# Optimization experiments

Hardware: AMD Instinct MI355X
Metric: run time of the kernel (lower is better)

The kernel has to match this reference:

```python
import jax, jax.numpy as jnp
import numpy as np
import math

B, S, D, H, FF, V, L = 8, 1024, 512, 8, 2048, 32000, 6
HD = D // H
EPS = 1e-6


def _positional_encoding(seq_len, d_model):
    pos = np.arange(seq_len, dtype=np.float32)[:, None]
    div = np.exp(np.arange(0, d_model, 2, dtype=np.float32) * (-math.log(10000.0) / d_model))
    pe = np.zeros((seq_len, d_model), dtype=np.float32)
    pe[:, 0::2] = np.sin(pos * div)
    pe[:, 1::2] = np.cos(pos * div)
    return jnp.asarray(pe)[None]  # [1, S, D]


def setup_inputs() -> dict:
    key = jax.random.key(0)
    ks = jax.random.split(key, 10)
    s = 0.02
    return {
        'tokens': jax.random.randint(ks[0], (B, S), 0, V, dtype=jnp.int32),
        'mask': jnp.ones((B, 1, 1, S), dtype=jnp.int32),
        'emb': jax.random.normal(ks[1], (V, D), jnp.float32) * s,
        'Wq': jax.random.normal(ks[2], (D, D), jnp.float32) * s,
        'bq': jnp.zeros((D,), jnp.float32),
        'Wk': jax.random.normal(ks[3], (D, D), jnp.float32) * s,
        'bk': jnp.zeros((D,), jnp.float32),
        'Wv': jax.random.normal(ks[4], (D, D), jnp.float32) * s,
        'bv': jnp.zeros((D,), jnp.float32),
        'Wo': jax.random.normal(ks[5], (D, D), jnp.float32) * s,
        'bo': jnp.zeros((D,), jnp.float32),
        'W1': jax.random.normal(ks[6], (D, FF), jnp.float32) * s,
        'b1': jnp.zeros((FF,), jnp.float32),
        'W2': jax.random.normal(ks[7], (FF, D), jnp.float32) * s,
        'b2': jnp.zeros((D,), jnp.float32),
        'ln_a1': jnp.ones((1,), jnp.float32),
        'ln_b1': jnp.zeros((1,), jnp.float32),
        'ln_a2': jnp.ones((1,), jnp.float32),
        'ln_b2': jnp.zeros((1,), jnp.float32),
    }


def _layernorm(x, alpha, bias):
    # custom LN from source: unbiased std (torch default), scalar alpha/bias,
    # eps added to std (not variance)
    mean = jnp.mean(x, axis=-1, keepdims=True)
    std = jnp.std(x, axis=-1, keepdims=True, ddof=1)
    return alpha * (x - mean) / (std + EPS) + bias


def reference(tokens, mask, emb, Wq, bq, Wk, bk, Wv, bv, Wo, bo,
              W1, b1, W2, b2, ln_a1, ln_b1, ln_a2, ln_b2):
    b, s = tokens.shape
    x = emb[tokens] * jnp.asarray(math.sqrt(D), emb.dtype)  # [B,S,D]
    x = x + _positional_encoding(s, D)
    neg = jnp.asarray(-1e9, x.dtype)
    scale = jnp.asarray(1.0 / math.sqrt(HD), x.dtype)
    # NOTE: source reuses the same EncoderBlock instance -> shared weights per layer
    for _ in range(L):
        # --- self-attention sublayer (pre-norm residual) ---
        h = _layernorm(x, ln_a1, ln_b1)
        q = (h @ Wq + bq).reshape(b, s, H, HD).transpose(0, 2, 1, 3)
        k = (h @ Wk + bk).reshape(b, s, H, HD).transpose(0, 2, 1, 3)
        v = (h @ Wv + bv).reshape(b, s, H, HD).transpose(0, 2, 1, 3)
        scores = jnp.einsum('bhqd,bhkd->bhqk', q, k) * scale
        scores = jnp.where(mask == 0, neg, scores)
        attn = jax.nn.softmax(scores, axis=-1)
        o = jnp.einsum('bhqk,bhkd->bhqd', attn, v)
        o = o.transpose(0, 2, 1, 3).reshape(b, s, D)
        x = x + (o @ Wo + bo)
        # --- feed-forward sublayer (pre-norm residual) ---
        h2 = _layernorm(x, ln_a2, ln_b2)
        x = x + (jax.nn.relu(h2 @ W1 + b1) @ W2 + b2)
    return x
```

## Files before the change

### kernel.cpp

```cpp
#include <hip/hip_runtime.h>
#include <hip/hip_bf16.h>
#include <math.h>

#define BB 8
#define SS 1024
#define DD 512
#define HH 8
#define FF 2048
#define LL 6
#define HD 64
#define MM (BB * SS)
#define EPS 1e-6f
#define QKVS 1536

typedef __attribute__((ext_vector_type(8))) short bf16x8;
typedef __attribute__((ext_vector_type(4))) float f32x4;

typedef __attribute__((address_space(1))) const unsigned int g_u32;
typedef __attribute__((address_space(3))) unsigned int l_u32;

__device__ __forceinline__ short f2bf(float f) {
    union { float f; unsigned u; } c; c.f = f;
    unsigned u = c.u;
    u += 0x7fff + ((u >> 16) & 1);
    return (short)(u >> 16);
}

__device__ __forceinline__ void gload_lds16(const void* g, void* l) {
    __builtin_amdgcn_global_load_lds((g_u32*)g, (l_u32*)l, 16, 0, 0);
}

#define SWZB(row, cb) (((row) * 128) + ((cb) ^ ((((row) & 7) ^ (((row) >> 3) & 7)) << 4)))

__global__ __launch_bounds__(256) void embed_pe_kernel(
    const int* __restrict__ tokens, const float* __restrict__ emb,
    float* __restrict__ x)
{
    int idx = blockIdx.x * 256 + threadIdx.x;
    int d  = idx & (DD - 1);
    int bs = idx >> 9;
    int s  = bs & (SS - 1);
    int tok = tokens[bs];
    float val = emb[(size_t)tok * DD + d] * 22.62741699796952f;
    int i2 = d & ~1;
    float freq = expf((float)i2 * -0.017988946039015984f);
    float ang = (float)s * freq;
    val += (d & 1) ? cosf(ang) : sinf(ang);
    x[idx] = val;
}

__global__ __launch_bounds__(256) void wcvt_kernel(
    const float* __restrict__ W, short* __restrict__ Wt, int K, int N)
{
    __shared__ float tile[32][33];
    int n0 = blockIdx.x * 32, k0 = blockIdx.y * 32;
    int tx = threadIdx.x & 31, ty = threadIdx.x >> 5;
    #pragma unroll
    for (int i = 0; i < 4; ++i)
        tile[ty + i * 8][tx] = W[(size_t)(k0 + ty + i * 8) * N + n0 + tx];
    __syncthreads();
    #pragma unroll
    for (int i = 0; i < 4; ++i)
        Wt[(size_t)(n0 + ty + i * 8) * K + k0 + tx] = f2bf(tile[tx][ty + i * 8]);
}

__global__ __launch_bounds__(256) void bcat_kernel(
    const float* __restrict__ bq, const float* __restrict__ bk,
    const float* __restrict__ bv, float* __restrict__ out)
{
    int i = blockIdx.x * 256 + threadIdx.x;
    float v = (i < 512) ? bq[i] : (i < 1024 ? bk[i - 512] : bv[i - 1024]);
    out[i] = v;
}

__global__ __launch_bounds__(256) void ln_kernel(
    const float* __restrict__ x, short* __restrict__ y,
    const float* __restrict__ alpha_p, const float* __restrict__ beta_p)
{
    int t = threadIdx.x;
    int wv = t >> 6, l = t & 63;
    int row = blockIdx.x * 4 + wv;
    const float* xr = x + (size_t)row * DD + l * 8;
    float4 a = *(const float4*)xr;
    float4 b = *(const float4*)(xr + 4);

    float v[8] = {a.x, a.y, a.z, a.w, b.x, b.y, b.z, b.w};
    float s = 0.0f;
    #pragma unroll
    for (int j = 0; j < 8; ++j) s += v[j];
    #pragma unroll
    for (int o = 32; o >= 1; o >>= 1) s += __shfl_xor(s, o, 64);
    float mean = s * (1.0f / 512.0f);

    float q = 0.0f;
    #pragma unroll
    for (int j = 0; j < 8; ++j) { v[j] -= mean; q += v[j] * v[j]; }
    #pragma unroll
    for (int o = 32; o >= 1; o >>= 1) q += __shfl_xor(q, o, 64);
    float stdv = sqrtf(q * (1.0f / 511.0f));

    float alpha = alpha_p[0], beta = beta_p[0];
    float inv = alpha / (stdv + EPS);
    bf16x8 ov;
    #pragma unroll
    for (int j = 0; j < 8; ++j) ov[j] = f2bf(v[j] * inv + beta);
    *(bf16x8*)(y + (size_t)row * DD + l * 8) = ov;
}

template <int BN, bool RELU, bool RES, bool OUT_BF16>
__global__ __launch_bounds__(256) void gemm_mfma(
    const short* __restrict__ A, const short* __restrict__ Wt,
    const float* __restrict__ bias, const float* __restrict__ R,
    void* __restrict__ Cout, int M, int N, int K)
{
    __shared__ __align__(16) short As[2][128 * 64];
    __shared__ __align__(16) short Bs[2][BN * 64];

    constexpr int MI = (BN == 128) ? 4 : 2;
    constexpr int NI = 4;

    const int t = threadIdx.x;
    const int w = t >> 6, l = t & 63;
    const int l15 = l & 15, l4 = l >> 4;
    const int wrow = (BN == 128) ? (w >> 1) * 64 : w * 32;
    const int wcol = (BN == 128) ? (w & 1) * 64 : 0;

    const int gx = gridDim.x;
    const int nwg = gx * gridDim.y;
    int id = blockIdx.y * gx + blockIdx.x;
    id = (id & 7) * (nwg >> 3) + (id >> 3);
    const int m0 = (id / gx) * 128, n0 = (id % gx) * BN;

    f32x4 acc[MI][NI];
    #pragma unroll
    for (int mi = 0; mi < MI; ++mi)
        #pragma unroll
        for (int ni = 0; ni < NI; ++ni) acc[mi][ni] = (f32x4){0.f, 0.f, 0.f, 0.f};

    const int lrow = l >> 3;
    const int lcol = (l & 7) * 8;

    auto stage = [&](int bufi, int k0) {
        #pragma unroll
        for (int i = 0; i < 4; ++i) {
            int r0 = (w * 4 + i) * 8;
            gload_lds16(A + (size_t)(m0 + r0 + lrow) * K + k0 + lcol,
                        &As[bufi][r0 * 64]);
        }
        #pragma unroll
        for (int i = 0; i < BN / 32; ++i) {
            int r0 = (w * (BN / 32) + i) * 8;
            gload_lds16(Wt + (size_t)(n0 + r0 + lrow) * K + k0 + lcol,
                        &Bs[bufi][r0 * 64]);
        }
    };

    const int NT = K >> 6;
    stage(0, 0);
    __syncthreads();

    int cur = 0;
    for (int tix = 0; tix < NT; ++tix) {
        if (tix + 1 < NT) stage(cur ^ 1, (tix + 1) * 64);

        #pragma unroll
        for (int ks = 0; ks < 2; ++ks) {
            bf16x8 af[MI], bf_[NI];
            #pragma unroll
            for (int mi = 0; mi < MI; ++mi)
                af[mi] = *(const bf16x8*)&As[cur][(wrow + mi * 16 + l15) * 64 + ks * 32 + l4 * 8];
            #pragma unroll
            for (int ni = 0; ni < NI; ++ni)
                bf_[ni] = *(const bf16x8*)&Bs[cur][(wcol + ni * 16 + l15) * 64 + ks * 32 + l4 * 8];
            #pragma unroll
            for (int mi = 0; mi < MI; ++mi)
                #pragma unroll
                for (int ni = 0; ni < NI; ++ni)
                    acc[mi][ni] = __builtin_amdgcn_mfma_f32_16x16x32_bf16(
                        af[mi], bf_[ni], acc[mi][ni], 0, 0, 0);
        }
        __syncthreads();
        cur ^= 1;
    }

    #pragma unroll
    for (int mi = 0; mi < MI; ++mi) {
        #pragma unroll
        for (int ni = 0; ni < NI; ++ni) {
            int col = n0 + wcol + ni * 16 + l15;
            float bcol = bias[col];
            #pragma unroll
            for (int r = 0; r < 4; ++r) {
                int row = m0 + wrow + mi * 16 + l4 * 4 + r;
                float c = acc[mi][ni][r] + bcol;
                if (RES)  c += R[(size_t)row * N + col];
                if (RELU) c = fmaxf(c, 0.0f);
                if (OUT_BF16) ((short*)Cout)[(size_t)row * N + col] = f2bf(c);
                else          ((float*)Cout)[(size_t)row * N + col] = c;
            }
        }
    }
}

__global__ __launch_bounds__(256) void attn_mfma_kernel(
    const short* __restrict__ qkv, const int* __restrict__ mask,
    short* __restrict__ o)
{
    __shared__ __align__(16) char Ks[64 * 128];
    __shared__ __align__(16) char Vt[64 * 128];
    __shared__ __align__(16) char Ps[4][32 * 128];

    const int qt = blockIdx.x;
    const int bh = blockIdx.y;
    const int b = bh >> 3, h = bh & 7;

    const int t = threadIdx.x;
    const int w = t >> 6;
    const int l = t & 63;
    const int l15 = l & 15, l4 = l >> 4;
    const int l7 = l & 7,  l8 = l >> 3;

    const short* kb = qkv + ((size_t)b * SS) * QKVS + 512 + h * HD;
    const short* vb = qkv + ((size_t)b * SS) * QKVS + 1024 + h * HD;
    const int*   mb = mask + (size_t)b * SS;
    const int qbase = qt * 128 + w * 32;

    bf16x8 qf[2][2];
    #pragma unroll
    for (int qs = 0; qs < 2; ++qs)
        #pragma unroll
        for (int ks = 0; ks < 2; ++ks)
            qf[qs][ks] = *(const bf16x8*)(qkv + ((size_t)b * SS + qbase + qs * 16 + l15) * QKVS
                                          + h * HD + ks * 32 + l4 * 8);

    bf16x8 onesv;
    #pragma unroll
    for (int j = 0; j < 8; ++j) onesv[j] = (short)0x3F80;

    float l_run[2][4];
    f32x4 O[2][4];
    #pragma unroll
    for (int qs = 0; qs < 2; ++qs) {
        #pragma unroll
        for (int r = 0; r < 4; ++r) l_run[qs][r] = 0.0f;
        #pragma unroll
        for (int ds = 0; ds < 4; ++ds) O[qs][ds] = (f32x4){0.f, 0.f, 0.f, 0.f};
    }

    char* Pw = Ps[w];
    const int par = l & 1;
    const int kr  = t >> 2;
    const int kcs = (t & 3) * 16;
    const int vkey0 = 16 * w + l7;
    const int vkey1 = 16 * w + 8 + l7;
    const int vd0 = 8 * l8;

    bf16x8 kreg0 = *(const bf16x8*)(kb + (size_t)kr * QKVS + kcs);
    bf16x8 kreg1 = *(const bf16x8*)(kb + (size_t)kr * QKVS + kcs + 8);
    int4   vreg0 = *(const int4*)(vb + (size_t)vkey0 * QKVS + vd0);
    int4   vreg1 = *(const int4*)(vb + (size_t)vkey1 * QKVS + vd0);

    for (int kt = 0; kt < SS / 64; ++kt) {
        *(bf16x8*)&Ks[SWZB(kr, kcs * 2)]      = kreg0;
        *(bf16x8*)&Ks[SWZB(kr, kcs * 2 + 16)] = kreg1;
        #pragma unroll
        for (int s = 0; s < 2; ++s) {
            int4 vv = s ? vreg1 : vreg0;
            int key = s ? vkey1 : vkey0;
            int p0 = __shfl_xor(vv.x, 1, 64);
            int p1 = __shfl_xor(vv.y, 1, 64);
            int p2 = __shfl_xor(vv.z, 1, 64);
            int p3 = __shfl_xor(vv.w, 1, 64);
            int cb = (key & ~1) * 2;
            int v0 = par ? (int)(((unsigned)p0 >> 16) | (vv.x & 0xFFFF0000))
                         : ((vv.x & 0xFFFF) | (p0 << 16));
            int v1 = par ? (int)(((unsigned)p1 >> 16) | (vv.y & 0xFFFF0000))
                         : ((vv.y & 0xFFFF) | (p1 << 16));
            int v2 = par ? (int)(((unsigned)p2 >> 16) | (vv.z & 0xFFFF0000))
                         : ((vv.z & 0xFFFF) | (p2 << 16));
            int v3 = par ? (int)(((unsigned)p3 >> 16) | (vv.w & 0xFFFF0000))
                         : ((vv.w & 0xFFFF) | (p3 << 16));
            *(int*)&Vt[SWZB(vd0 + 0 + par, cb)] = v0;
            *(int*)&Vt[SWZB(vd0 + 2 + par, cb)] = v1;
            *(int*)&Vt[SWZB(vd0 + 4 + par, cb)] = v2;
            *(int*)&Vt[SWZB(vd0 + 6 + par, cb)] = v3;
        }
        __syncthreads();

        if (kt + 1 < SS / 64) {
            const short* kbn = kb + (size_t)((kt + 1) * 64) * QKVS;
            const short* vbn = vb + (size_t)((kt + 1) * 64) * QKVS;
            kreg0 = *(const bf16x8*)(kbn + (size_t)kr * QKVS + kcs);
            kreg1 = *(const bf16x8*)(kbn + (size_t)kr * QKVS + kcs + 8);
            vreg0 = *(const int4*)(vbn + (size_t)vkey0 * QKVS + vd0);
            vreg1 = *(const int4*)(vbn + (size_t)vkey1 * QKVS + vd0);
        }

        f32x4 S[2][4];
        #pragma unroll
        for (int qs = 0; qs < 2; ++qs)
            #pragma unroll
            for (int ku = 0; ku < 4; ++ku) S[qs][ku] = (f32x4){0.f, 0.f, 0.f, 0.f};
        #pragma unroll
        for (int ks = 0; ks < 2; ++ks) {
            bf16x8 kf[4];
            #pragma unroll
            for (int ku = 0; ku < 4; ++ku)
                kf[ku] = *(const bf16x8*)&Ks[SWZB(ku * 16 + l15, ks * 64 + l4 * 16)];
            #pragma unroll
            for (int qs = 0; qs < 2; ++qs)
                #pragma unroll
                for (int ku = 0; ku < 4; ++ku)
                    S[qs][ku] = __builtin_amdgcn_mfma_f32_16x16x32_bf16(
                        qf[qs][ks], kf[ku], S[qs][ku], 0, 0, 0);
        }

        int mv[4];
        #pragma unroll
        for (int ku = 0; ku < 4; ++ku) mv[ku] = mb[kt * 64 + ku * 16 + l15];

        #pragma unroll
        for (int qs = 0; qs < 2; ++qs)
            #pragma unroll
            for (int ku = 0; ku < 4; ++ku)
                #pragma unroll
                for (int r = 0; r < 4; ++r) {
                    float sv = (mv[ku] == 0) ? -1e9f : S[qs][ku][r] * 0.125f;
                    *(short*)&Pw[SWZB(qs * 16 + l4 * 4 + r, (ku * 16 + l15) * 2)]
                        = f2bf(__expf(sv));
                }

        #pragma unroll
        for (int qs = 0; qs < 2; ++qs) {
            bf16x8 pf[2];
            #pragma unroll
            for (int ks = 0; ks < 2; ++ks)
                pf[ks] = *(const bf16x8*)&Pw[SWZB(qs * 16 + l15, ks * 64 + l4 * 16)];

            f32x4 rs = (f32x4){0.f, 0.f, 0.f, 0.f};
            rs = __builtin_amdgcn_mfma_f32_16x16x32_bf16(pf[0], onesv, rs, 0, 0, 0);
            rs = __builtin_amdgcn_mfma_f32_16x16x32_bf16(pf[1], onesv, rs, 0, 0, 0);
            #pragma unroll
            for (int r = 0; r < 4; ++r) l_run[qs][r] += rs[r];

            #pragma unroll
            for (int ks = 0; ks < 2; ++ks) {
                bf16x8 vf[4];
                #pragma unroll
                for (int ds = 0; ds < 4; ++ds)
                    vf[ds] = *(const bf16x8*)&Vt[SWZB(ds * 16 + l15, ks * 64 + l4 * 16)];
                #pragma unroll
                for (int ds = 0; ds < 4; ++ds)
                    O[qs][ds] = __builtin_amdgcn_mfma_f32_16x16x32_bf16(
                        pf[ks], vf[ds], O[qs][ds], 0, 0, 0);
            }
        }
        __syncthreads();
    }

    #pragma unroll
    for (int qs = 0; qs < 2; ++qs)
        #pragma unroll
        for (int r = 0; r < 4; ++r) {
            float inv = 1.0f / l_run[qs][r];
            int qrow = qbase + qs * 16 + l4 * 4 + r;
            short* orow = o + ((size_t)b * SS + qrow) * DD + h * HD;
            #pragma unroll
            for (int ds = 0; ds < 4; ++ds)
                orow[ds * 16 + l15] = f2bf(O[qs][ds][r] * inv);
        }
}

extern "C" void kernel_launch(void* const* d_in, const int* in_sizes, int n_in,
                              void* d_out, int out_size, void* d_ws, size_t ws_size,
                              hipStream_t stream)
{
    const int*   tokens = (const int*)  d_in[0];
    const int*   mask   = (const int*)  d_in[1];
    const float* emb    = (const float*)d_in[2];
    const float* Wq     = (const float*)d_in[3];
    const float* bq     = (const float*)d_in[4];
    const float* Wk     = (const float*)d_in[5];
    const float* bk     = (const float*)d_in[6];
    const float* Wv     = (const float*)d_in[7];
    const float* bv     = (const float*)d_in[8];
    const float* Wo     = (const float*)d_in[9];
    const float* bo     = (const float*)d_in[10];
    const float* W1     = (const float*)d_in[11];
    const float* b1     = (const float*)d_in[12];
    const float* W2     = (const float*)d_in[13];
    const float* b2     = (const float*)d_in[14];
    const float* ln_a1  = (const float*)d_in[15];
    const float* ln_b1  = (const float*)d_in[16];
    const float* ln_a2  = (const float*)d_in[17];
    const float* ln_b2  = (const float*)d_in[18];

    float* x = (float*)d_out;

    char* p = (char*)d_ws;
    short* qkv  = (short*)p;  p += (size_t)MM * QKVS * 2;
    short* h    = (short*)p;  p += (size_t)MM * DD * 2;
    short* ff   = (short*)p;  p += (size_t)MM * FF * 2;
    short* Wqkvt= (short*)p;  p += (size_t)QKVS * DD * 2;
    short* Wot  = (short*)p;  p += (size_t)DD * DD * 2;
    short* W1t  = (short*)p;  p += (size_t)FF * DD * 2;
    short* W2t  = (short*)p;  p += (size_t)DD * FF * 2;
    float* bqkv = (float*)p;  p += QKVS * 4;

    embed_pe_kernel<<<(MM * DD) / 256, 256, 0, stream>>>(tokens, emb, x);

    wcvt_kernel<<<dim3(DD / 32, DD / 32), 256, 0, stream>>>(Wq, Wqkvt,            DD, DD);
    wcvt_kernel<<<dim3(DD / 32, DD / 32), 256, 0, stream>>>(Wk, Wqkvt + 512*512,  DD, DD);
    wcvt_kernel<<<dim3(DD / 32, DD / 32), 256, 0, stream>>>(Wv, Wqkvt + 1024*512, DD, DD);
    wcvt_kernel<<<dim3(DD / 32, DD / 32), 256, 0, stream>>>(Wo, Wot, DD, DD);
    wcvt_kernel<<<dim3(FF / 32, DD / 32), 256, 0, stream>>>(W1, W1t, DD, FF);
    wcvt_kernel<<<dim3(DD / 32, FF / 32), 256, 0, stream>>>(W2, W2t, FF, DD);
    bcat_kernel<<<QKVS / 256, 256, 0, stream>>>(bq, bk, bv, bqkv);

    dim3 gQKV(QKVS / 128, MM / 128);
    dim3 gO  (DD / 64,    MM / 128);
    dim3 gF1 (FF / 128,   MM / 128);
    dim3 gF2 (DD / 64,    MM / 128);
    dim3 gA  (SS / 128,   BB * HH);

    for (int layer = 0; layer < LL; ++layer) {
        ln_kernel<<<MM / 4, 256, 0, stream>>>(x, h, ln_a1, ln_b1);
        gemm_mfma<128, false, false, true><<<gQKV, 256, 0, stream>>>(
            h, Wqkvt, bqkv, nullptr, qkv, MM, QKVS, DD);
        attn_mfma_kernel<<<gA, 256, 0, stream>>>(qkv, mask, h);
        gemm_mfma<64, false, true, false><<<gO, 256, 0, stream>>>(
            h, Wot, bo, x, x, MM, DD, DD);

        ln_kernel<<<MM / 4, 256, 0, stream>>>(x, h, ln_a2, ln_b2);
        gemm_mfma<128, true, false, true><<<gF1, 256, 0, stream>>>(
            h, W1t, b1, nullptr, ff, MM, FF, DD);
        gemm_mfma<64, false, true, false><<<gF2, 256, 0, stream>>>(
            ff, W2t, b2, x, x, MM, DD, FF);
    }
}
```

Measured before the change: 1.199 ms.

## Use partial vmcnt waits in GEMM, 512-thread attention blocks, exp2 softmax

The GEMM main loop now replaces the full __syncthreads with explicit s_waitcnt vmcnt waits and raw barriers, so the prefetch of the next tile can stay in flight while the current tile is computed. The attention kernel doubles to 8 waves per block covering 256 queries, which halves redundant K/V tile loads per query and gives each thread a single K/V load per tile. Softmax switches to exp2f with a folded log2(e) scale, and bf16 conversion uses the HIP intrinsic. The hand-counted vmcnt values must match the actual number of outstanding loads, otherwise LDS reads could race with data still arriving.

```diff
diff --git a/kernel.cpp b/kernel.cpp
--- a/kernel.cpp
+++ b/kernel.cpp
@@ -20,14 +20,24 @@
 typedef __attribute__((address_space(3))) unsigned int l_u32;
 
 __device__ __forceinline__ short f2bf(float f) {
-    union { float f; unsigned u; } c; c.f = f;
-    unsigned u = c.u;
-    u += 0x7fff + ((u >> 16) & 1);
-    return (short)(u >> 16);
+    __hip_bfloat16 h = __float2bfloat16(f);
+    return *reinterpret_cast<short*>(&h);
 }
 
 __device__ __forceinline__ void gload_lds16(const void* g, void* l) {
     __builtin_amdgcn_global_load_lds((g_u32*)g, (l_u32*)l, 16, 0, 0);
+}
+
+template <int NN> __device__ __forceinline__ void wait_vm() {
+    if constexpr (NN == 8)      asm volatile("s_waitcnt vmcnt(8)" ::: "memory");
+    else if constexpr (NN == 6) asm volatile("s_waitcnt vmcnt(6)" ::: "memory");
+    else                        asm volatile("s_waitcnt vmcnt(0)" ::: "memory");
+}
+
+__device__ __forceinline__ void barrier_mem() {
+    asm volatile("" ::: "memory");
+    __builtin_amdgcn_s_barrier();
+    asm volatile("" ::: "memory");
 }
 
 #define SWZB(row, cb) (((row) * 128) + ((cb) ^ ((((row) & 7) ^ (((row) >> 3) & 7)) << 4)))
@@ -118,6 +128,7 @@
 
     constexpr int MI = (BN == 128) ? 4 : 2;
     constexpr int NI = 4;
+    constexpr int LB = (BN == 128) ? 8 : 6;
 
     const int t = threadIdx.x;
     const int w = t >> 6, l = t & 63;
@@ -157,11 +168,16 @@
 
     const int NT = K >> 6;
     stage(0, 0);
-    __syncthreads();
 
     int cur = 0;
     for (int tix = 0; tix < NT; ++tix) {
-        if (tix + 1 < NT) stage(cur ^ 1, (tix + 1) * 64);
+        if (tix + 1 < NT) {
+            stage(cur ^ 1, (tix + 1) * 64);
+            wait_vm<LB>();
+        } else {
+            wait_vm<0>();
+        }
+        barrier_mem();
 
         #pragma unroll
         for (int ks = 0; ks < 2; ++ks) {
@@ -179,7 +195,7 @@
                     acc[mi][ni] = __builtin_amdgcn_mfma_f32_16x16x32_bf16(
                         af[mi], bf_[ni], acc[mi][ni], 0, 0, 0);
         }
-        __syncthreads();
+        barrier_mem();
         cur ^= 1;
     }
 
@@ -202,13 +218,13 @@
     }
 }
 
-__global__ __launch_bounds__(256) void attn_mfma_kernel(
+__global__ __launch_bounds__(512) void attn_mfma_kernel(
     const short* __restrict__ qkv, const int* __restrict__ mask,
     short* __restrict__ o)
 {
     __shared__ __align__(16) char Ks[64 * 128];
     __shared__ __align__(16) char Vt[64 * 128];
-    __shared__ __align__(16) char Ps[4][32 * 128];
+    __shared__ __align__(16) char Ps[8][32 * 128];
 
     const int qt = blockIdx.x;
     const int bh = blockIdx.y;
@@ -223,7 +239,7 @@
     const short* kb = qkv + ((size_t)b * SS) * QKVS + 512 + h * HD;
     const short* vb = qkv + ((size_t)b * SS) * QKVS + 1024 + h * HD;
     const int*   mb = mask + (size_t)b * SS;
-    const int qbase = qt * 128 + w * 32;
+    const int qbase = qt * 256 + w * 32;
 
     bf16x8 qf[2][2];
     #pragma unroll
@@ -249,29 +265,25 @@
 
     char* Pw = Ps[w];
     const int par = l & 1;
-    const int kr  = t >> 2;
-    const int kcs = (t & 3) * 16;
-    const int vkey0 = 16 * w + l7;
-    const int vkey1 = 16 * w + 8 + l7;
-    const int vd0 = 8 * l8;
-
-    bf16x8 kreg0 = *(const bf16x8*)(kb + (size_t)kr * QKVS + kcs);
-    bf16x8 kreg1 = *(const bf16x8*)(kb + (size_t)kr * QKVS + kcs + 8);
-    int4   vreg0 = *(const int4*)(vb + (size_t)vkey0 * QKVS + vd0);
-    int4   vreg1 = *(const int4*)(vb + (size_t)vkey1 * QKVS + vd0);
+    const int kr  = t >> 3;
+    const int kcs = (t & 7) * 8;
+    const int vkey = 8 * w + l7;
+    const int vd0  = 8 * l8;
+
+    bf16x8 kreg = *(const bf16x8*)(kb + (size_t)kr * QKVS + kcs);
+    int4   vreg = *(const int4*)(vb + (size_t)vkey * QKVS + vd0);
+
+    const float SC = 0.18033688011112042f;
 
     for (int kt = 0; kt < SS / 64; ++kt) {
-        *(bf16x8*)&Ks[SWZB(kr, kcs * 2)]      = kreg0;
-        *(bf16x8*)&Ks[SWZB(kr, kcs * 2 + 16)] = kreg1;
-        #pragma unroll
-        for (int s = 0; s < 2; ++s) {
-            int4 vv = s ? vreg1 : vreg0;
-            int key = s ? vkey1 : vkey0;
+        *(bf16x8*)&Ks[SWZB(kr, kcs * 2)] = kreg;
+        {
+            int4 vv = vreg;
             int p0 = __shfl_xor(vv.x, 1, 64);
             int p1 = __shfl_xor(vv.y, 1, 64);
             int p2 = __shfl_xor(vv.z, 1, 64);
             int p3 = __shfl_xor(vv.w, 1, 64);
-            int cb = (key & ~1) * 2;
+            int cb = (vkey & ~1) * 2;
             int v0 = par ? (int)(((unsigned)p0 >> 16) | (vv.x & 0xFFFF0000))
                          : ((vv.x & 0xFFFF) | (p0 << 16));
             int v1 = par ? (int)(((unsigned)p1 >> 16) | (vv.y & 0xFFFF0000))
@@ -290,10 +302,8 @@
         if (kt + 1 < SS / 64) {
             const short* kbn = kb + (size_t)((kt + 1) * 64) * QKVS;
             const short* vbn = vb + (size_t)((kt + 1) * 64) * QKVS;
-            kreg0 = *(const bf16x8*)(kbn + (size_t)kr * QKVS + kcs);
-            kreg1 = *(const bf16x8*)(kbn + (size_t)kr * QKVS + kcs + 8);
-            vreg0 = *(const int4*)(vbn + (size_t)vkey0 * QKVS + vd0);
-            vreg1 = *(const int4*)(vbn + (size_t)vkey1 * QKVS + vd0);
+            kreg = *(const bf16x8*)(kbn + (size_t)kr * QKVS + kcs);
+            vreg = *(const int4*)(vbn + (size_t)vkey * QKVS + vd0);
         }
 
         f32x4 S[2][4];
@@ -325,9 +335,9 @@
             for (int ku = 0; ku < 4; ++ku)
                 #pragma unroll
                 for (int r = 0; r < 4; ++r) {
-                    float sv = (mv[ku] == 0) ? -1e9f : S[qs][ku][r] * 0.125f;
+                    float sv = (mv[ku] == 0) ? -1e9f : S[qs][ku][r] * SC;
                     *(short*)&Pw[SWZB(qs * 16 + l4 * 4 + r, (ku * 16 + l15) * 2)]
-                        = f2bf(__expf(sv));
+                        = f2bf(exp2f(sv));
                 }
 
         #pragma unroll
@@ -421,13 +431,13 @@
     dim3 gO  (DD / 64,    MM / 128);
     dim3 gF1 (FF / 128,   MM / 128);
     dim3 gF2 (DD / 64,    MM / 128);
-    dim3 gA  (SS / 128,   BB * HH);
+    dim3 gA  (SS / 256,   BB * HH);
 
     for (int layer = 0; layer < LL; ++layer) {
         ln_kernel<<<MM / 4, 256, 0, stream>>>(x, h, ln_a1, ln_b1);
         gemm_mfma<128, false, false, true><<<gQKV, 256, 0, stream>>>(
             h, Wqkvt, bqkv, nullptr, qkv, MM, QKVS, DD);
-        attn_mfma_kernel<<<gA, 256, 0, stream>>>(qkv, mask, h);
+        attn_mfma_kernel<<<gA, 512, 0, stream>>>(qkv, mask, h);
         gemm_mfma<64, false, true, false><<<gO, 256, 0, stream>>>(
             h, Wot, bo, x, x, MM, DD, DD);
 
```

Result: slower. 1.238 ms (+3.3%).
